# Optimization experiments

Measured on AMD Instinct MI355X. Metric: run time of the kernel, lower is better.

Reference implementation:

```python
import jax, jax.numpy as jnp
import numpy as np

B, L, C = 32, 1024, 32     # batch, seq_len, enc_in
D = 512                     # d_model / hidden_size
SEG = 16                    # seg_len
K = 25                      # moving_avg kernel
SX = L // SEG               # seg_num_x = 64 sequential GRU steps
PRED = 16                   # pred_len == seg_len -> seg_num_y = 1


def setup_inputs() -> dict:
    key = jax.random.key(0)
    ks = jax.random.split(key, 20)
    r = lambda i, shape: jax.random.normal(ks[i], shape, dtype=jnp.float32) * 0.05
    return {
        "x": jax.random.normal(ks[0], (B, L, C), dtype=jnp.float32),
        "W_emb": r(1, (D, SEG)), "b_emb": r(2, (D,)),
        "Wih_s": r(3, (3 * D, D)), "Whh_s": r(4, (3 * D, D)),
        "bih_s": r(5, (3 * D,)), "bhh_s": r(6, (3 * D,)),
        "Wih_t": r(7, (3 * D, D)), "Whh_t": r(8, (3 * D, D)),
        "bih_t": r(9, (3 * D,)), "bhh_t": r(10, (3 * D,)),
        "pos_s": r(11, (1, D // 2)), "ch_s": r(12, (C, D // 2)),
        "pos_t": r(13, (1, D // 2)), "ch_t": r(14, (C, D // 2)),
        "Wps": r(15, (SEG, D)), "bps": r(16, (SEG,)),
        "Wpt": r(17, (SEG, D)), "bpt": r(18, (SEG,)),
    }


def _moving_mean(x, k):
    # Autoformer moving_avg over dim 1 with edge replication (length preserved, k odd)
    pad = (k - 1) // 2
    xp = jnp.concatenate([jnp.repeat(x[:, :1], pad, 1), x, jnp.repeat(x[:, -1:], pad, 1)], axis=1)
    cs = jnp.cumsum(xp, axis=1)
    cs = jnp.concatenate([jnp.zeros_like(cs[:, :1]), cs], axis=1)
    return (cs[:, k:] - cs[:, :-k]) / k


def _gru_cell(x, h, Wih, Whh, bih, bhh):
    gi = x @ Wih.T + bih
    gh = h @ Whh.T + bhh
    ir, iz, in_ = jnp.split(gi, 3, axis=-1)
    hr, hz, hn = jnp.split(gh, 3, axis=-1)
    r = jax.nn.sigmoid(ir + hr)
    z = jax.nn.sigmoid(iz + hz)
    n = jnp.tanh(in_ + r * hn)
    return (1.0 - z) * n + z * h


def _forward(x, W_emb, b_emb, Wih_s, Whh_s, bih_s, bhh_s, Wih_t, Whh_t, bih_t, bhh_t,
             pos_s, ch_s, pos_t, ch_t, Wps, bps, Wpt, bpt):
    seq_last = jax.lax.stop_gradient(x[:, -1:, :])          # (B,1,C), detached
    xc = (x - seq_last).transpose(0, 2, 1)                  # (B,C,L)
    mean = _moving_mean(xc, K)                              # trend
    xs = xc - mean                                          # seasonal residual
    xt = mean
    # value embedding: (B*C, SX, SEG) -> (B*C, SX, D), ReLU
    xs = jax.nn.relu(xs.reshape(-1, SX, SEG) @ W_emb.T + b_emb)
    xt = jax.nn.relu(xt.reshape(-1, SX, SEG) @ W_emb.T + b_emb)
    N = B * C
    h0 = jnp.zeros((N, D), x.dtype)

    def step(carry, inp):
        hs, ht = carry
        xs_i, xt_i = inp
        hs = _gru_cell(xs_i, hs, Wih_s, Whh_s, bih_s, bhh_s)
        ht = _gru_cell(xt_i, ht, Wih_t, Whh_t, bih_t, bhh_t)
        return (hs, ht), None

    (hs, ht), _ = jax.lax.scan(step, (h0, h0), (xs.transpose(1, 0, 2), xt.transpose(1, 0, 2)))

    # decoder (seg_num_y == 1): pos/channel embedding -> one more GRUCell step
    pe_s = jnp.tile(jnp.concatenate([jnp.broadcast_to(pos_s, (C, D // 2)), ch_s], -1), (B, 1))  # (B*C,D)
    pe_t = jnp.tile(jnp.concatenate([jnp.broadcast_to(pos_t, (C, D // 2)), ch_t], -1), (B, 1))
    hs2 = _gru_cell(pe_s, hs, Wih_s, Whh_s, bih_s, bhh_s)
    ht2 = _gru_cell(pe_t, ht, Wih_t, Whh_t, bih_t, bhh_t)
    # predict heads (dropout is identity in eval)
    y = ht2 @ Wpt.T + bpt + hs2 @ Wps.T + bps               # (B*C, SEG)
    y = y.reshape(B, C, PRED).transpose(0, 2, 1)            # (B, PRED, C)
    return y + seq_last


def reference(x, W_emb, b_emb, Wih_s, Whh_s, bih_s, bhh_s, Wih_t, Whh_t, bih_t, bhh_t,
              pos_s, ch_s, pos_t, ch_t, Wps, bps, Wpt, bpt):
    return _forward(x, W_emb, b_emb, Wih_s, Whh_s, bih_s, bhh_s, Wih_t, Whh_t, bih_t, bhh_t,
                    pos_s, ch_s, pos_t, ch_t, Wps, bps, Wpt, bpt)
```

## Files before the change

kernel.cpp:

```cpp
#include <hip/hip_runtime.h>
#include <math.h>

#define B_   32
#define L_   1024
#define C_   32
#define D_   512
#define SEG_ 16
#define SX_  64
#define N_   1024

typedef _Float16 f16x8 __attribute__((ext_vector_type(8)));
typedef _Float16 f16x4 __attribute__((ext_vector_type(4)));
typedef float    f32x4 __attribute__((ext_vector_type(4)));

__device__ __forceinline__ void stage16(const void* g, void* l) {
    __builtin_amdgcn_global_load_lds((const __attribute__((address_space(1))) void*)g,
                                     (__attribute__((address_space(3))) void*)l, 16, 0, 0);
}
__device__ __forceinline__ void stage16l(const void* g, void* l) {
    __builtin_amdgcn_global_load_lds((const __attribute__((address_space(1))) void*)g,
                                     (__attribute__((address_space(3))) void*)l, 16, 0, 1);
}
__device__ __forceinline__ void store_v4_sc0(void* p, f16x8 v) {
    asm volatile("global_store_dwordx4 %0, %1, off sc0" :: "v"(p), "v"(v) : "memory");
}
__device__ __forceinline__ float fsig(float x) {
    return __builtin_amdgcn_rcpf(1.f + __expf(-x));
}
__device__ __forceinline__ float ftanh(float x) {
    return 1.f - 2.f * __builtin_amdgcn_rcpf(1.f + __expf(2.f * x));
}

__global__ __launch_bounds__(256) void prep_kernel(const float* __restrict__ x,
                                                   float* __restrict__ xs_seg,
                                                   float* __restrict__ xt_seg) {
    int b = blockIdx.x >> 2;
    int t = ((blockIdx.x & 3) << 8) + threadIdx.x;
    const float* xb    = x + (size_t)b * (L_ * C_);
    const float* xrow  = xb + (size_t)t * C_;
    const float* xlast = xb + (size_t)(L_ - 1) * C_;

    float diff[C_];
#pragma unroll
    for (int c = 0; c < C_; ++c) diff[c] = xrow[c] - xlast[c];
    float ps[C_ + 1];
    ps[0] = 0.f;
#pragma unroll
    for (int c = 0; c < C_; ++c) ps[c + 1] = ps[c] + diff[c];

    int s = t >> 4, q = t & 15;
#pragma unroll
    for (int c = 0; c < C_; ++c) {
        int lo = c - 12, hi = c + 12;
        float sum = ps[(hi < 31 ? hi : 31) + 1] - ps[lo > 0 ? lo : 0];
        if (lo < 0)  sum += (float)(-lo)     * diff[0];
        if (hi > 31) sum += (float)(hi - 31) * diff[31];
        float mean = sum * (1.0f / 25.0f);
        size_t idx = ((size_t)s * N_ + (size_t)(b * C_ + c)) * SEG_ + q;
        xt_seg[idx] = mean;
        xs_seg[idx] = diff[c] - mean;
    }
}

__global__ __launch_bounds__(256) void emb_kernel(
    const float* __restrict__ xs_seg, const float* __restrict__ xt_seg,
    const float* __restrict__ W_emb, const float* __restrict__ b_emb,
    _Float16* __restrict__ emb_buf, int s0) {
    int bid = blockIdx.x;
    int gru = bid >> 8, sl = (bid >> 4) & 15, nch = bid & 15;
    int step = s0 + sl, n0 = nch * 64;
    const float* xseg = gru ? xt_seg : xs_seg;
    __shared__ float xl[64 * 16];
    int tid = threadIdx.x;
    const float* src = xseg + ((size_t)step * N_ + n0) * SEG_;
    for (int i = tid; i < 1024; i += 256) xl[i] = src[i];

    int kg = tid & 127;
    int rh = tid >> 7;
    float w[4][16], bb[4];
#pragma unroll
    for (int i = 0; i < 4; ++i) {
        int k = kg * 4 + i;
        const float4* wr = (const float4*)(W_emb + (size_t)k * 16);
#pragma unroll
        for (int v = 0; v < 4; ++v) {
            float4 tt = wr[v];
            w[i][v * 4 + 0] = tt.x; w[i][v * 4 + 1] = tt.y;
            w[i][v * 4 + 2] = tt.z; w[i][v * 4 + 3] = tt.w;
        }
        bb[i] = b_emb[k];
    }
    __syncthreads();
    _Float16* dst = emb_buf + ((size_t)(sl * 2 + gru) * N_ + n0) * D_ + kg * 4;
    for (int r = 0; r < 32; ++r) {
        int row = rh * 32 + r;
        float a0 = bb[0], a1 = bb[1], a2 = bb[2], a3 = bb[3];
#pragma unroll
        for (int q = 0; q < 16; ++q) {
            float xv = xl[row * 16 + q];
            a0 = fmaf(xv, w[0][q], a0);
            a1 = fmaf(xv, w[1][q], a1);
            a2 = fmaf(xv, w[2][q], a2);
            a3 = fmaf(xv, w[3][q], a3);
        }
        f16x4 v;
        v[0] = (_Float16)(a0 > 0.f ? a0 : 0.f);
        v[1] = (_Float16)(a1 > 0.f ? a1 : 0.f);
        v[2] = (_Float16)(a2 > 0.f ? a2 : 0.f);
        v[3] = (_Float16)(a3 > 0.f ? a3 : 0.f);
        *(f16x4*)(dst + (size_t)row * D_) = v;
    }
}

__global__ __launch_bounds__(256) void pack_wih_kernel(
    const float* __restrict__ Wih_s, const float* __restrict__ Wih_t,
    _Float16* __restrict__ wp) {
    int e = blockIdx.x * 256 + threadIdx.x;
    int kk = e & 31;
    int t = e >> 5;
    int gc = t % 1536;
    int t2 = t / 1536;
    int kt = t2 & 15, gru = t2 >> 4;
    int member = gc / 192, r = gc % 192;
    int wn = r / 48, r2 = r % 48;
    int gate = r2 >> 4, jl = r2 & 15;
    int j = member * 64 + wn * 16 + jl;
    int k = kt * 32 + kk;
    const float* W = gru ? Wih_t : Wih_s;
    wp[e] = (_Float16)W[(size_t)(gate * 512 + j) * 512 + k];
}

__global__ __launch_bounds__(256) void pack_whh5_kernel(
    const float* __restrict__ Whh_s, const float* __restrict__ Whh_t,
    _Float16* __restrict__ wp) {
    int e = blockIdx.x * 256 + threadIdx.x;
    int fi = e & 7;
    int t = e >> 3;
    int c = t % 3072;
    int t2 = t / 3072;
    int kt = t2 & 3;
    int t3 = t2 >> 2;
    int member = t3 & 7, gru = t3 >> 3;
    int gc = c >> 4, s = c & 15;
    int q = s ^ (gc & 15);
    int k = kt * 128 + q * 8 + fi;
    int wn = gc / 48, r2 = gc % 48;
    int gate = r2 >> 4, jl = r2 & 15;
    int j = member * 64 + wn * 16 + jl;
    const float* W = gru ? Whh_t : Whh_s;
    wp[e] = (_Float16)W[(size_t)(gate * 512 + j) * 512 + k];
}

__global__ __launch_bounds__(256) void pack_pe_kernel(
    const float* __restrict__ pos_s, const float* __restrict__ ch_s,
    const float* __restrict__ pos_t, const float* __restrict__ ch_t,
    _Float16* __restrict__ pe) {
    int e = blockIdx.x * 256 + threadIdx.x;
    int k = e & 511;
    int n = (e >> 9) & 1023;
    int gru = e >> 19;
    int c = n & 31;
    const float* pos = gru ? pos_t : pos_s;
    const float* ch  = gru ? ch_t  : ch_s;
    float v = (k < 256) ? pos[k] : ch[c * 256 + (k - 256)];
    pe[e] = (_Float16)v;
}

__global__ __launch_bounds__(512, 2) void gi_gemm_kernel(
    const _Float16* __restrict__ emb, const _Float16* __restrict__ pe,
    const _Float16* __restrict__ wih_pack,
    _Float16* __restrict__ gi, _Float16* __restrict__ gi_pe, int mode) {
    __shared__ __align__(16) char smem[53248];
    char* sA = smem;
    char* sB = smem + 8192;
    int Mt = blockIdx.x & 7, Nt = blockIdx.x >> 3;
    int sl = blockIdx.y, gru = blockIdx.z;
    int tid = threadIdx.x, w = tid >> 6, lane = tid & 63;
    int wm = w & 1, wn = w >> 1, ml = lane & 15, qq = lane >> 4;

    const char* Ab = mode ? (const char*)(pe  + (size_t)gru * N_ * D_)
                          : (const char*)(emb + (size_t)(sl * 2 + gru) * N_ * D_);
    const char* Bb = (const char*)wih_pack + (size_t)gru * 16 * 1536 * 64
                     + (size_t)Nt * 192 * 64;

    int rA = tid >> 2, kqA = (tid & 3) ^ ((rA >> 1) & 3);
    const char* gA = Ab + (size_t)(Mt * 128 + rA) * 1024 + kqA * 16;
    int g1 = tid >> 2, kq1 = (tid & 3) ^ ((g1 >> 1) & 3);
    int c2 = 512 + tid, g2 = c2 >> 2, kq2 = (c2 & 3) ^ ((g2 >> 1) & 3);

    int offA[4], offB[3];
#pragma unroll
    for (int mf = 0; mf < 4; ++mf) {
        int row = wm * 64 + mf * 16 + ml;
        offA[mf] = (row * 4 + (qq ^ ((row >> 1) & 3))) * 16;
    }
#pragma unroll
    for (int g = 0; g < 3; ++g) {
        int gc = wn * 48 + g * 16 + ml;
        offB[g] = (gc * 4 + (qq ^ ((gc >> 1) & 3))) * 16;
    }

    f32x4 acc[4][3];
#pragma unroll
    for (int mf = 0; mf < 4; ++mf)
#pragma unroll
        for (int g = 0; g < 3; ++g) {
            f32x4 z = {0.f, 0.f, 0.f, 0.f};
            acc[mf][g] = z;
        }

    for (int kt = 0; kt < 16; ++kt) {
        __syncthreads();
        stage16(gA + kt * 64, sA + w * 1024);
        const char* Bkt = Bb + (size_t)kt * (1536 * 64);
        stage16(Bkt + g1 * 64 + kq1 * 16, sB + w * 1024);
        if (w < 4) stage16(Bkt + g2 * 64 + kq2 * 16, sB + 8192 + w * 1024);
        asm volatile("s_waitcnt vmcnt(0)" ::: "memory");
        __syncthreads();
        f16x8 a[4];
#pragma unroll
        for (int mf = 0; mf < 4; ++mf) a[mf] = *(const f16x8*)(sA + offA[mf]);
#pragma unroll
        for (int g = 0; g < 3; ++g) {
            f16x8 b = *(const f16x8*)(sB + offB[g]);
#pragma unroll
            for (int mf = 0; mf < 4; ++mf)
                acc[mf][g] = __builtin_amdgcn_mfma_f32_16x16x32_f16(a[mf], b, acc[mf][g], 0, 0, 0);
        }
    }

    __syncthreads();
#pragma unroll
    for (int mf = 0; mf < 4; ++mf) {
        int wm_c = mf >> 1, rt = mf & 1;
        int tid_c = (wn * 2 + wm_c) * 64 + qq * 16 + ml;
        char* base = smem + wm * 26624 + tid_c * 52;
#pragma unroll
        for (int g = 0; g < 3; ++g)
#pragma unroll
            for (int reg = 0; reg < 4; ++reg) {
                int v = rt * 12 + reg * 3 + g;
                *(_Float16*)(base + v * 2) = (_Float16)acc[mf][g][reg];
            }
    }
    __syncthreads();
    _Float16* ob = mode ? gi_pe + (size_t)gru * 8 * 16 * 512 * 24
                        : gi    + (size_t)(sl * 2 + gru) * 8 * 16 * 512 * 24;
    char* obB = (char*)ob;
#pragma unroll
    for (int s = 0; s < 6; ++s) {
        int o = tid * 16 + s * 8192;
        int mc = o / 24576;
        int o2 = o - mc * 24576;
        int tc = o2 / 48;
        int r  = o2 - tc * 48;
        const char* src = smem + mc * 26624 + tc * 52 + r;
        int4 val;
        val.x = *(const int*)(src);
        val.y = *(const int*)(src + 4);
        val.z = *(const int*)(src + 8);
        val.w = *(const int*)(src + 12);
        *(int4*)(obB + (size_t)(Nt * 16 + Mt * 2 + mc) * 24576 + o2) = val;
    }
}

__global__ __launch_bounds__(512) void gru_chain_kernel(
    const _Float16* __restrict__ whh_pk5,
    const _Float16* __restrict__ gi_base,
    const float* __restrict__ bih_s, const float* __restrict__ bhh_s,
    const float* __restrict__ bih_t, const float* __restrict__ bhh_t,
    _Float16* __restrict__ hbf0, _Float16* __restrict__ hbf1,
    unsigned* __restrict__ flags, int nsteps, int sbase) {
    __shared__ __align__(16) char sA[65536];
    __shared__ __align__(16) char sEx[49152];
    int bid = blockIdx.x;
    int member = bid >> 5, chain = bid & 31;
    int Mt = chain & 15, gru = chain >> 4;
    int tid = threadIdx.x, w = tid >> 6, lane = tid & 63;
    int ml = lane & 15, qq = lane >> 4;
    int km = w & 1, wn = w >> 1;

    const char* h0 = (const char*)hbf0 + ((size_t)gru * N_ + Mt * 64) * 1024;
    const char* h1 = (const char*)hbf1 + ((size_t)gru * N_ + Mt * 64) * 1024;

    f16x8 bfr[3][8];
    {
        const _Float16* Wb = whh_pk5 + (size_t)(gru * 8 + member) * 4 * 24576;
#pragma unroll
        for (int g = 0; g < 3; ++g) {
            int gc = wn * 48 + g * 16 + ml;
#pragma unroll
            for (int ks = 0; ks < 8; ++ks) {
                int kt = km * 2 + (ks >> 2);
                int q8 = ((ks & 3) * 4 + qq) ^ (gc & 15);
                bfr[g][ks] = *(const f16x8*)(Wb + (size_t)kt * 24576
                                             + (size_t)(gc * 16 + q8) * 8);
            }
        }
    }

    int cS0 = (lane & 48) | ((lane & 15) ^ (w & 15));
    int cS1 = (lane & 48) | ((lane & 15) ^ ((w + 8) & 15));

    int offR[4], cp[8];
#pragma unroll
    for (int rt = 0; rt < 4; ++rt) offR[rt] = (rt * 16 + ml) * 1024;
#pragma unroll
    for (int ks = 0; ks < 8; ++ks) {
        int c = km * 32 + ks * 4 + qq;
        cp[ks] = ((c & 48) | ((c & 15) ^ ml)) * 16;
    }

    const float* bi = gru ? bih_t : bih_s;
    const float* bh = gru ? bhh_t : bhh_s;
    int j = member * 64 + wn * 16 + ml;
    float bir = bi[j], biz = bi[D_ + j], bin = bi[2 * D_ + j];
    float bhr = bh[j], bhz = bh[D_ + j], bhn = bh[2 * D_ + j];
    float hp[2][4];
#pragma unroll
    for (int rtL = 0; rtL < 2; ++rtL)
#pragma unroll
        for (int reg = 0; reg < 4; ++reg) {
            int row = Mt * 64 + km * 32 + rtL * 16 + qq * 4 + reg;
            hp[rtL][reg] = (float)hbf0[((size_t)gru * N_ + row) * D_ + j];
        }

    unsigned* fbase = flags + chain * 256;
    const _Float16* giTid0 = gi_base
        + (((size_t)gru * 8 + member) * 16 + Mt) * 512 * 24 + (size_t)tid * 24;
    size_t giStep = (size_t)2 * 8 * 16 * 512 * 24;

    int dir0 = sbase & 1;
    f16x8 gv0, gv1, gv2;
    {
        const _Float16* gp = giTid0;
        gv0 = *(const f16x8*)(gp);
        gv1 = *(const f16x8*)(gp + 8);
        gv2 = *(const f16x8*)(gp + 16);
        const char* hin = dir0 ? h1 : h0;
#pragma unroll
        for (int r = 0; r < 8; ++r) {
            int row = r * 8 + w;
            stage16l(hin + (size_t)row * 1024 + (size_t)((r & 1) ? cS1 : cS0) * 16,
                     sA + row * 1024);
        }
    }

    for (int it = 0; it < nsteps; ++it) {
        int gstep = sbase + it;
        _Float16* hout = (gstep & 1) ? hbf0 : hbf1;

        f32x4 acc[4][3];
#pragma unroll
        for (int rt = 0; rt < 4; ++rt)
#pragma unroll
            for (int g = 0; g < 3; ++g) {
                f32x4 z = {0.f, 0.f, 0.f, 0.f};
                acc[rt][g] = z;
            }

        asm volatile("s_waitcnt vmcnt(0)" ::: "memory");
        __syncthreads();

#pragma unroll
        for (int ks = 0; ks < 8; ++ks) {
            f16x8 a0 = *(const f16x8*)(sA + offR[0] + cp[ks]);
            f16x8 a1 = *(const f16x8*)(sA + offR[1] + cp[ks]);
            f16x8 a2 = *(const f16x8*)(sA + offR[2] + cp[ks]);
            f16x8 a3 = *(const f16x8*)(sA + offR[3] + cp[ks]);
#pragma unroll
            for (int g = 0; g < 3; ++g) {
                acc[0][g] = __builtin_amdgcn_mfma_f32_16x16x32_f16(a0, bfr[g][ks], acc[0][g], 0, 0, 0);
                acc[1][g] = __builtin_amdgcn_mfma_f32_16x16x32_f16(a1, bfr[g][ks], acc[1][g], 0, 0, 0);
                acc[2][g] = __builtin_amdgcn_mfma_f32_16x16x32_f16(a2, bfr[g][ks], acc[2][g], 0, 0, 0);
                acc[3][g] = __builtin_amdgcn_mfma_f32_16x16x32_f16(a3, bfr[g][ks], acc[3][g], 0, 0, 0);
            }
        }

        char* exw = sEx + (size_t)(wn * 64 + lane) * 16;
        if (km == 0) {
#pragma unroll
            for (int g = 0; g < 3; ++g) {
                *(f32x4*)(exw + (size_t)(6 + g) * 4096) = acc[2][g];
                *(f32x4*)(exw + (size_t)(9 + g) * 4096) = acc[3][g];
            }
        } else {
#pragma unroll
            for (int g = 0; g < 3; ++g) {
                *(f32x4*)(exw + (size_t)(0 + g) * 4096) = acc[0][g];
                *(f32x4*)(exw + (size_t)(3 + g) * 4096) = acc[1][g];
            }
        }
        __syncthreads();
        f32x4 s0[3], s1[3];
        if (km == 0) {
#pragma unroll
            for (int g = 0; g < 3; ++g) {
                s0[g] = acc[0][g] + *(const f32x4*)(exw + (size_t)(0 + g) * 4096);
                s1[g] = acc[1][g] + *(const f32x4*)(exw + (size_t)(3 + g) * 4096);
            }
        } else {
#pragma unroll
            for (int g = 0; g < 3; ++g) {
                s0[g] = acc[2][g] + *(const f32x4*)(exw + (size_t)(6 + g) * 4096);
                s1[g] = acc[3][g] + *(const f32x4*)(exw + (size_t)(9 + g) * 4096);
            }
        }

        char* sH = sA;
        int colb = (wn * 16 + ml) * 2;
#pragma unroll
        for (int reg = 0; reg < 4; ++reg) {
            int v0 = reg * 3;
            float gr = (float)((v0 + 0) < 8 ? gv0[(v0 + 0) & 7]
                      : ((v0 + 0) < 16 ? gv1[(v0 + 0) & 7] : gv2[(v0 + 0) & 7]));
            float gz = (float)((v0 + 1) < 8 ? gv0[(v0 + 1) & 7]
                      : ((v0 + 1) < 16 ? gv1[(v0 + 1) & 7] : gv2[(v0 + 1) & 7]));
            float gn = (float)((v0 + 2) < 8 ? gv0[(v0 + 2) & 7]
                      : ((v0 + 2) < 16 ? gv1[(v0 + 2) & 7] : gv2[(v0 + 2) & 7]));
            float r = fsig(s0[0][reg] + gr + bir + bhr);
            float z = fsig(s0[1][reg] + gz + biz + bhz);
            float nn = ftanh(gn + bin + r * (s0[2][reg] + bhn));
            float hv = (1.f - z) * nn + z * hp[0][reg];
            hp[0][reg] = hv;
            int rl = km * 32 + qq * 4 + reg;
            *(_Float16*)(sH + rl * 144 + colb) = (_Float16)hv;
        }
#pragma unroll
        for (int reg = 0; reg < 4; ++reg) {
            int v0 = 12 + reg * 3;
            float gr = (float)((v0 + 0) < 8 ? gv0[(v0 + 0) & 7]
                      : ((v0 + 0) < 16 ? gv1[(v0 + 0) & 7] : gv2[(v0 + 0) & 7]));
            float gz = (float)((v0 + 1) < 8 ? gv0[(v0 + 1) & 7]
                      : ((v0 + 1) < 16 ? gv1[(v0 + 1) & 7] : gv2[(v0 + 1) & 7]));
            float gn = (float)((v0 + 2) < 8 ? gv0[(v0 + 2) & 7]
                      : ((v0 + 2) < 16 ? gv1[(v0 + 2) & 7] : gv2[(v0 + 2) & 7]));
            float r = fsig(s1[0][reg] + gr + bir + bhr);
            float z = fsig(s1[1][reg] + gz + biz + bhz);
            float nn = ftanh(gn + bin + r * (s1[2][reg] + bhn));
            float hv = (1.f - z) * nn + z * hp[1][reg];
            hp[1][reg] = hv;
            int rl = km * 32 + 16 + qq * 4 + reg;
            *(_Float16*)(sH + rl * 144 + colb) = (_Float16)hv;
        }
        __syncthreads();
        {
            int srow = tid >> 3, spart = tid & 7;
            f16x8 hv8 = *(const f16x8*)(sH + srow * 144 + spart * 16);
            _Float16* gdst = hout + ((size_t)gru * N_ + Mt * 64 + srow) * D_
                             + member * 64 + spart * 8;
            store_v4_sc0(gdst, hv8);
        }

        asm volatile("s_waitcnt vmcnt(0)" ::: "memory");
        __syncthreads();
        if (tid == 0)
            __hip_atomic_store(fbase + member * 32, (unsigned)(gstep + 1),
                               __ATOMIC_RELAXED, __HIP_MEMORY_SCOPE_AGENT);

        if (it < nsteps - 1) {
            const _Float16* gp = giTid0 + (size_t)(it + 1) * giStep;
            gv0 = *(const f16x8*)(gp);
            gv1 = *(const f16x8*)(gp + 8);
            gv2 = *(const f16x8*)(gp + 16);
            if (w == 0) {
                const unsigned* fp = fbase + (lane & 7) * 32;
                unsigned tgt = (unsigned)(gstep + 1);
                int guard = 0;
                while (true) {
                    unsigned v = __hip_atomic_load(fp, __ATOMIC_RELAXED,
                                                   __HIP_MEMORY_SCOPE_AGENT);
                    if (__all(v >= tgt)) break;
                    __builtin_amdgcn_s_sleep(1);
                    if (++guard > (1 << 20)) break;
                }
            }
            __syncthreads();
            const char* hinN = ((gstep + 1) & 1) ? h1 : h0;
#pragma unroll
            for (int r = 0; r < 8; ++r) {
                int row = r * 8 + w;
                stage16l(hinN + (size_t)row * 1024 + (size_t)((r & 1) ? cS1 : cS0) * 16,
                         sA + row * 1024);
            }
        }
    }
}

__global__ __launch_bounds__(256) void head_kernel(
    const _Float16* __restrict__ hs2, const _Float16* __restrict__ ht2,
    const float* __restrict__ Wps, const float* __restrict__ bps,
    const float* __restrict__ Wpt, const float* __restrict__ bpt,
    const float* __restrict__ x, float* __restrict__ out) {
    int g = blockIdx.x * 256 + threadIdx.x;
    int n = g >> 4, p = g & 15;
    int b = n >> 5, c = n & 31;
    const _Float16* hs = hs2 + (size_t)n * D_;
    const _Float16* ht = ht2 + (size_t)n * D_;
    const float* ws = Wps + (size_t)p * D_;
    const float* wt = Wpt + (size_t)p * D_;
    float acc = bps[p] + bpt[p];
    for (int k = 0; k < D_; ++k)
        acc += (float)hs[k] * ws[k] + (float)ht[k] * wt[k];
    float last = x[((size_t)b * L_ + (L_ - 1)) * C_ + c];
    out[((size_t)b * SEG_ + p) * C_ + c] = acc + last;
}

extern "C" void kernel_launch(void* const* d_in, const int* in_sizes, int n_in,
                              void* d_out, int out_size, void* d_ws, size_t ws_size,
                              hipStream_t stream) {
    const float* x     = (const float*)d_in[0];
    const float* W_emb = (const float*)d_in[1];
    const float* b_emb = (const float*)d_in[2];
    const float* Wih_s = (const float*)d_in[3];
    const float* Whh_s = (const float*)d_in[4];
    const float* bih_s = (const float*)d_in[5];
    const float* bhh_s = (const float*)d_in[6];
    const float* Wih_t = (const float*)d_in[7];
    const float* Whh_t = (const float*)d_in[8];
    const float* bih_t = (const float*)d_in[9];
    const float* bhh_t = (const float*)d_in[10];
    const float* pos_s = (const float*)d_in[11];
    const float* ch_s  = (const float*)d_in[12];
    const float* pos_t = (const float*)d_in[13];
    const float* ch_t  = (const float*)d_in[14];
    const float* Wps   = (const float*)d_in[15];
    const float* bps   = (const float*)d_in[16];
    const float* Wpt   = (const float*)d_in[17];
    const float* bpt   = (const float*)d_in[18];
    float* out = (float*)d_out;

    char* p = (char*)d_ws;
    float* xs_seg = (float*)p;          p += (size_t)SX_ * N_ * SEG_ * 4;
    float* xt_seg = (float*)p;          p += (size_t)SX_ * N_ * SEG_ * 4;
    _Float16* emb_buf = (_Float16*)p;   p += (size_t)16 * 2 * N_ * D_ * 2;
    _Float16* gi_buf  = (_Float16*)p;   p += (size_t)16 * 2 * 8 * 16 * 512 * 24 * 2;
    _Float16* gi_pe   = (_Float16*)p;   p += (size_t)2 * 8 * 16 * 512 * 24 * 2;
    _Float16* pe_buf  = (_Float16*)p;   p += (size_t)2 * N_ * D_ * 2;
    _Float16* wih_pk  = (_Float16*)p;   p += (size_t)2 * 16 * 1536 * 32 * 2;
    _Float16* whh_pk5 = (_Float16*)p;   p += (size_t)2 * 8 * 4 * 3072 * 8 * 2;
    _Float16* hbf0 = (_Float16*)p;      p += (size_t)2 * N_ * D_ * 2;
    _Float16* hbf1 = (_Float16*)p;      p += (size_t)2 * N_ * D_ * 2;
    unsigned* flags = (unsigned*)p;     p += 32 * 256 * 4;

    hipMemsetAsync(hbf0, 0, (size_t)2 * N_ * D_ * 2, stream);
    hipMemsetAsync(flags, 0, 32 * 256 * 4, stream);

    pack_wih_kernel<<<6144, 256, 0, stream>>>(Wih_s, Wih_t, wih_pk);
    pack_whh5_kernel<<<6144, 256, 0, stream>>>(Whh_s, Whh_t, whh_pk5);
    pack_pe_kernel<<<4096, 256, 0, stream>>>(pos_s, ch_s, pos_t, ch_t, pe_buf);
    prep_kernel<<<B_ * 4, 256, 0, stream>>>(x, xs_seg, xt_seg);

    for (int b = 0; b < 4; ++b) {
        emb_kernel<<<512, 256, 0, stream>>>(xs_seg, xt_seg, W_emb, b_emb, emb_buf, b * 16);
        gi_gemm_kernel<<<dim3(64, 16, 2), 512, 0, stream>>>(
            emb_buf, pe_buf, wih_pk, gi_buf, gi_pe, 0);
        gru_chain_kernel<<<256, 512, 0, stream>>>(
            whh_pk5, gi_buf, bih_s, bhh_s, bih_t, bhh_t,
            hbf0, hbf1, flags, 16, b * 16);
    }
    gi_gemm_kernel<<<dim3(64, 1, 2), 512, 0, stream>>>(
        emb_buf, pe_buf, wih_pk, gi_buf, gi_pe, 1);
    gru_chain_kernel<<<256, 512, 0, stream>>>(
        whh_pk5, gi_pe, bih_s, bhh_s, bih_t, bhh_t,
        hbf0, hbf1, flags, 1, 64);

    head_kernel<<<N_ * SEG_ / 256, 256, 0, stream>>>(
        hbf1, hbf1 + (size_t)N_ * D_, Wps, bps, Wpt, bpt, x, out);
}
```

Before: 773.5 us.

## Merge setup kernels, prefetch next-step gate inputs, alias GRU smem, swap GEMM tile order

Folds the three weight/PE packing kernels and the decomposition prep kernel into one launch, removing three launches and their gaps. In the GRU chain kernel, the next step's input-gate values are now loaded right after the barrier so the global load overlaps the recurrent MMA. The exchange buffer is aliased onto the staging shared memory to shrink LDS, with an extra barrier added to keep the reuse safe. The gi GEMM block index mapping is swapped so adjacent blocks share the same A tile instead of the same weight tile.

```diff
diff --git a/kernel.cpp b/kernel.cpp
--- a/kernel.cpp
+++ b/kernel.cpp
@@ -31,34 +31,83 @@
     return 1.f - 2.f * __builtin_amdgcn_rcpf(1.f + __expf(2.f * x));
 }
 
-__global__ __launch_bounds__(256) void prep_kernel(const float* __restrict__ x,
-                                                   float* __restrict__ xs_seg,
-                                                   float* __restrict__ xt_seg) {
-    int b = blockIdx.x >> 2;
-    int t = ((blockIdx.x & 3) << 8) + threadIdx.x;
-    const float* xb    = x + (size_t)b * (L_ * C_);
-    const float* xrow  = xb + (size_t)t * C_;
-    const float* xlast = xb + (size_t)(L_ - 1) * C_;
-
-    float diff[C_];
-#pragma unroll
-    for (int c = 0; c < C_; ++c) diff[c] = xrow[c] - xlast[c];
-    float ps[C_ + 1];
-    ps[0] = 0.f;
-#pragma unroll
-    for (int c = 0; c < C_; ++c) ps[c + 1] = ps[c] + diff[c];
-
-    int s = t >> 4, q = t & 15;
-#pragma unroll
-    for (int c = 0; c < C_; ++c) {
-        int lo = c - 12, hi = c + 12;
-        float sum = ps[(hi < 31 ? hi : 31) + 1] - ps[lo > 0 ? lo : 0];
-        if (lo < 0)  sum += (float)(-lo)     * diff[0];
-        if (hi > 31) sum += (float)(hi - 31) * diff[31];
-        float mean = sum * (1.0f / 25.0f);
-        size_t idx = ((size_t)s * N_ + (size_t)(b * C_ + c)) * SEG_ + q;
-        xt_seg[idx] = mean;
-        xs_seg[idx] = diff[c] - mean;
+__global__ __launch_bounds__(256) void setup_kernel(
+    const float* __restrict__ x, float* __restrict__ xs_seg, float* __restrict__ xt_seg,
+    const float* __restrict__ Wih_s, const float* __restrict__ Wih_t,
+    _Float16* __restrict__ wih_pk,
+    const float* __restrict__ Whh_s, const float* __restrict__ Whh_t,
+    _Float16* __restrict__ whh_pk5,
+    const float* __restrict__ pos_s, const float* __restrict__ ch_s,
+    const float* __restrict__ pos_t, const float* __restrict__ ch_t,
+    _Float16* __restrict__ pe) {
+    int bid = blockIdx.x, tid = threadIdx.x;
+    if (bid < 6144) {
+        int e = bid * 256 + tid;
+        int kk = e & 31;
+        int t = e >> 5;
+        int gc = t % 1536;
+        int t2 = t / 1536;
+        int kt = t2 & 15, gru = t2 >> 4;
+        int member = gc / 192, r = gc % 192;
+        int wn = r / 48, r2 = r % 48;
+        int gate = r2 >> 4, jl = r2 & 15;
+        int j = member * 64 + wn * 16 + jl;
+        int k = kt * 32 + kk;
+        const float* W = gru ? Wih_t : Wih_s;
+        wih_pk[e] = (_Float16)W[(size_t)(gate * 512 + j) * 512 + k];
+    } else if (bid < 12288) {
+        int e = (bid - 6144) * 256 + tid;
+        int fi = e & 7;
+        int t = e >> 3;
+        int c = t % 3072;
+        int t2 = t / 3072;
+        int kt = t2 & 3;
+        int t3 = t2 >> 2;
+        int member = t3 & 7, gru = t3 >> 3;
+        int gc = c >> 4, s = c & 15;
+        int q = s ^ (gc & 15);
+        int k = kt * 128 + q * 8 + fi;
+        int wn = gc / 48, r2 = gc % 48;
+        int gate = r2 >> 4, jl = r2 & 15;
+        int j = member * 64 + wn * 16 + jl;
+        const float* W = gru ? Whh_t : Whh_s;
+        whh_pk5[e] = (_Float16)W[(size_t)(gate * 512 + j) * 512 + k];
+    } else if (bid < 16384) {
+        int e = (bid - 12288) * 256 + tid;
+        int k = e & 511;
+        int n = (e >> 9) & 1023;
+        int gru = e >> 19;
+        int c = n & 31;
+        const float* pos = gru ? pos_t : pos_s;
+        const float* ch  = gru ? ch_t  : ch_s;
+        float v = (k < 256) ? pos[k] : ch[c * 256 + (k - 256)];
+        pe[e] = (_Float16)v;
+    } else {
+        int b2 = bid - 16384;
+        int b = b2 >> 2;
+        int t = ((b2 & 3) << 8) + tid;
+        const float* xb    = x + (size_t)b * (L_ * C_);
+        const float* xrow  = xb + (size_t)t * C_;
+        const float* xlast = xb + (size_t)(L_ - 1) * C_;
+        float diff[C_];
+#pragma unroll
+        for (int c = 0; c < C_; ++c) diff[c] = xrow[c] - xlast[c];
+        float ps[C_ + 1];
+        ps[0] = 0.f;
+#pragma unroll
+        for (int c = 0; c < C_; ++c) ps[c + 1] = ps[c] + diff[c];
+        int s = t >> 4, q = t & 15;
+#pragma unroll
+        for (int c = 0; c < C_; ++c) {
+            int lo = c - 12, hi = c + 12;
+            float sum = ps[(hi < 31 ? hi : 31) + 1] - ps[lo > 0 ? lo : 0];
+            if (lo < 0)  sum += (float)(-lo)     * diff[0];
+            if (hi > 31) sum += (float)(hi - 31) * diff[31];
+            float mean = sum * (1.0f / 25.0f);
+            size_t idx = ((size_t)s * N_ + (size_t)(b * C_ + c)) * SEG_ + q;
+            xt_seg[idx] = mean;
+            xs_seg[idx] = diff[c] - mean;
+        }
     }
 }
 
@@ -112,60 +161,6 @@
     }
 }
 
-__global__ __launch_bounds__(256) void pack_wih_kernel(
-    const float* __restrict__ Wih_s, const float* __restrict__ Wih_t,
-    _Float16* __restrict__ wp) {
-    int e = blockIdx.x * 256 + threadIdx.x;
-    int kk = e & 31;
-    int t = e >> 5;
-    int gc = t % 1536;
-    int t2 = t / 1536;
-    int kt = t2 & 15, gru = t2 >> 4;
-    int member = gc / 192, r = gc % 192;
-    int wn = r / 48, r2 = r % 48;
-    int gate = r2 >> 4, jl = r2 & 15;
-    int j = member * 64 + wn * 16 + jl;
-    int k = kt * 32 + kk;
-    const float* W = gru ? Wih_t : Wih_s;
-    wp[e] = (_Float16)W[(size_t)(gate * 512 + j) * 512 + k];
-}
-
-__global__ __launch_bounds__(256) void pack_whh5_kernel(
-    const float* __restrict__ Whh_s, const float* __restrict__ Whh_t,
-    _Float16* __restrict__ wp) {
-    int e = blockIdx.x * 256 + threadIdx.x;
-    int fi = e & 7;
-    int t = e >> 3;
-    int c = t % 3072;
-    int t2 = t / 3072;
-    int kt = t2 & 3;
-    int t3 = t2 >> 2;
-    int member = t3 & 7, gru = t3 >> 3;
-    int gc = c >> 4, s = c & 15;
-    int q = s ^ (gc & 15);
-    int k = kt * 128 + q * 8 + fi;
-    int wn = gc / 48, r2 = gc % 48;
-    int gate = r2 >> 4, jl = r2 & 15;
-    int j = member * 64 + wn * 16 + jl;
-    const float* W = gru ? Whh_t : Whh_s;
-    wp[e] = (_Float16)W[(size_t)(gate * 512 + j) * 512 + k];
-}
-
-__global__ __launch_bounds__(256) void pack_pe_kernel(
-    const float* __restrict__ pos_s, const float* __restrict__ ch_s,
-    const float* __restrict__ pos_t, const float* __restrict__ ch_t,
-    _Float16* __restrict__ pe) {
-    int e = blockIdx.x * 256 + threadIdx.x;
-    int k = e & 511;
-    int n = (e >> 9) & 1023;
-    int gru = e >> 19;
-    int c = n & 31;
-    const float* pos = gru ? pos_t : pos_s;
-    const float* ch  = gru ? ch_t  : ch_s;
-    float v = (k < 256) ? pos[k] : ch[c * 256 + (k - 256)];
-    pe[e] = (_Float16)v;
-}
-
 __global__ __launch_bounds__(512, 2) void gi_gemm_kernel(
     const _Float16* __restrict__ emb, const _Float16* __restrict__ pe,
     const _Float16* __restrict__ wih_pack,
@@ -173,7 +168,7 @@
     __shared__ __align__(16) char smem[53248];
     char* sA = smem;
     char* sB = smem + 8192;
-    int Mt = blockIdx.x & 7, Nt = blockIdx.x >> 3;
+    int Nt = blockIdx.x & 7, Mt = blockIdx.x >> 3;
     int sl = blockIdx.y, gru = blockIdx.z;
     int tid = threadIdx.x, w = tid >> 6, lane = tid & 63;
     int wm = w & 1, wn = w >> 1, ml = lane & 15, qq = lane >> 4;
@@ -271,8 +266,9 @@
     const float* __restrict__ bih_t, const float* __restrict__ bhh_t,
     _Float16* __restrict__ hbf0, _Float16* __restrict__ hbf1,
     unsigned* __restrict__ flags, int nsteps, int sbase) {
-    __shared__ __align__(16) char sA[65536];
-    __shared__ __align__(16) char sEx[49152];
+    __shared__ __align__(16) char smem[65536];
+    char* sA = smem;
+    char* sEx = smem + 16384;
     int bid = blockIdx.x;
     int member = bid >> 5, chain = bid & 31;
     int Mt = chain & 15, gru = chain >> 4;
@@ -362,6 +358,13 @@
         asm volatile("s_waitcnt vmcnt(0)" ::: "memory");
         __syncthreads();
 
+        int itn = (it + 1 < nsteps) ? it + 1 : it;
+        const _Float16* gpn = giTid0 + (size_t)itn * giStep;
+        f16x8 ngv0 = *(const f16x8*)(gpn);
+        f16x8 ngv1 = *(const f16x8*)(gpn + 8);
+        f16x8 ngv2 = *(const f16x8*)(gpn + 16);
+        __builtin_amdgcn_sched_barrier(0);
+
 #pragma unroll
         for (int ks = 0; ks < 8; ++ks) {
             f16x8 a0 = *(const f16x8*)(sA + offR[0] + cp[ks]);
@@ -377,6 +380,7 @@
             }
         }
 
+        __syncthreads();
         char* exw = sEx + (size_t)(wn * 64 + lane) * 16;
         if (km == 0) {
 #pragma unroll
@@ -459,10 +463,6 @@
                                __ATOMIC_RELAXED, __HIP_MEMORY_SCOPE_AGENT);
 
         if (it < nsteps - 1) {
-            const _Float16* gp = giTid0 + (size_t)(it + 1) * giStep;
-            gv0 = *(const f16x8*)(gp);
-            gv1 = *(const f16x8*)(gp + 8);
-            gv2 = *(const f16x8*)(gp + 16);
             if (w == 0) {
                 const unsigned* fp = fbase + (lane & 7) * 32;
                 unsigned tgt = (unsigned)(gstep + 1);
@@ -484,6 +484,7 @@
                          sA + row * 1024);
             }
         }
+        gv0 = ngv0; gv1 = ngv1; gv2 = ngv2;
     }
 }
 
@@ -546,10 +547,9 @@
     hipMemsetAsync(hbf0, 0, (size_t)2 * N_ * D_ * 2, stream);
     hipMemsetAsync(flags, 0, 32 * 256 * 4, stream);
 
-    pack_wih_kernel<<<6144, 256, 0, stream>>>(Wih_s, Wih_t, wih_pk);
-    pack_whh5_kernel<<<6144, 256, 0, stream>>>(Whh_s, Whh_t, whh_pk5);
-    pack_pe_kernel<<<4096, 256, 0, stream>>>(pos_s, ch_s, pos_t, ch_t, pe_buf);
-    prep_kernel<<<B_ * 4, 256, 0, stream>>>(x, xs_seg, xt_seg);
+    setup_kernel<<<16512, 256, 0, stream>>>(
+        x, xs_seg, xt_seg, Wih_s, Wih_t, wih_pk, Whh_s, Whh_t, whh_pk5,
+        pos_s, ch_s, pos_t, ch_t, pe_buf);
 
     for (int b = 0; b < 4; ++b) {
         emb_kernel<<<512, 256, 0, stream>>>(xs_seg, xt_seg, W_emb, b_emb, emb_buf, b * 16);
```

Result: slower. 809.9 us (+4.7%).
